# Kernel tuning notes

Hardware: AMD Instinct MI355X
Metric: run time of the kernel (lower is better)

The kernel has to match this reference:

```python
import jax, jax.numpy as jnp
import numpy as np

D_MODEL = 1024
HEAD = 16


def setup_inputs() -> dict:
    key = jax.random.key(0)
    ks = jax.random.split(key, 11)
    B, S, D = 2, 2048, D_MODEL
    s = 1.0 / np.sqrt(D)
    return {
        "query": jax.random.normal(ks[0], (B, S, D), jnp.float32),
        "value": jax.random.normal(ks[1], (B, S, D), jnp.float32),
        "key": jax.random.normal(ks[2], (B, S, D), jnp.float32),
        "Wq_w": jax.random.normal(ks[3], (D, D), jnp.float32) * s,
        "Wq_b": jnp.zeros((D,), jnp.float32),
        "Wk_w": jax.random.normal(ks[4], (D, D), jnp.float32) * s,
        "Wk_b": jnp.zeros((D,), jnp.float32),
        "Wv_w": jax.random.normal(ks[5], (D, D), jnp.float32) * s,
        "Wv_b": jnp.zeros((D,), jnp.float32),
        "Wo_w": jax.random.normal(ks[6], (D, D), jnp.float32) * s,
        "Wo_b": jnp.zeros((D,), jnp.float32),
    }


def reference(query, value, key, Wq_w, Wq_b, Wk_w, Wk_b, Wv_w, Wv_b, Wo_w, Wo_b):
    B, S, D = query.shape
    H = HEAD
    kd = D // H
    # Linear projections (torch Linear: x @ W.T + b)
    Q = query @ Wq_w.T + Wq_b
    K = key @ Wk_w.T + Wk_b
    V = value @ Wv_w.T + Wv_b
    # [B, S, D] -> [B, H, S, kd]
    Q = Q.reshape(B, S, H, kd).transpose(0, 2, 1, 3)
    K = K.reshape(B, S, H, kd).transpose(0, 2, 1, 3)
    V = V.reshape(B, S, H, kd).transpose(0, 2, 1, 3)
    scale = 1.0 / jnp.sqrt(jnp.asarray(kd, query.dtype))
    score = jnp.einsum("bhqd,bhkd->bhqk", Q, K) * scale  # [B,H,S,S]
    attn = jax.nn.softmax(score, axis=-1)
    x = jnp.einsum("bhqk,bhkd->bhqd", attn, V)  # [B,H,S,kd]
    x = x.transpose(0, 2, 1, 3).reshape(B, S, D)
    return x @ Wo_w.T + Wo_b
```

## Files before the change

### kernel.cpp

```cpp
#include <hip/hip_runtime.h>
#include <stdint.h>
#include <stddef.h>


typedef __attribute__((ext_vector_type(8))) short short8;
typedef __attribute__((ext_vector_type(4))) float floatx4;
typedef __attribute__((ext_vector_type(16))) float f32x16;
typedef __attribute__((ext_vector_type(4))) unsigned short ushort4v;

#define MFMA16(a, b, c) __builtin_amdgcn_mfma_f32_16x16x32_bf16((a), (b), (c), 0, 0, 0)
#define MFMA32(a, b, c) __builtin_amdgcn_mfma_f32_32x32x16_bf16((a), (b), (c), 0, 0, 0)

#define CL2 0.18033688011112042f

__device__ __forceinline__ unsigned short f2bf(float f) {
  union { float f; unsigned u; } v; v.f = f;
  unsigned u = v.u;
  return (unsigned short)((u + 0x7fffu + ((u >> 16) & 1u)) >> 16);
}

__device__ __forceinline__ float fast_exp2(float x) {
  float r;
  asm("v_exp_f32 %0, %1" : "=v"(r) : "v"(x));
  return r;
}

__device__ __forceinline__ unsigned cvt_pk_bf16(float lo, float hi) {
  unsigned r;
  asm("v_cvt_pk_bf16_f32 %0, %1, %2" : "=v"(r) : "v"(lo), "v"(hi));
  return r;
}

#define PSWAP(a, b) asm("v_permlane32_swap_b32 %0, %1" : "+v"(a), "+v"(b))

#define WAITBAR(N) do { \
  asm volatile("s_waitcnt vmcnt(" #N ")" ::: "memory"); \
  __builtin_amdgcn_s_barrier(); \
  __builtin_amdgcn_sched_barrier(0); \
} while (0)

union B8 { unsigned short s[8]; short8 v; };
union U4 { unsigned w[4]; short8 v; };

__device__ __forceinline__ void gload_lds16(const unsigned short* g, unsigned short* l) {
  __builtin_amdgcn_global_load_lds(
      (__attribute__((address_space(1))) void*)(g),
      (__attribute__((address_space(3))) void*)(l), 16, 0, 0);
}

__global__ __launch_bounds__(256) void convert_all(
    const float* __restrict__ q, const float* __restrict__ k, const float* __restrict__ v,
    const float* __restrict__ wq, const float* __restrict__ wk,
    const float* __restrict__ wv, const float* __restrict__ wo,
    unsigned short* __restrict__ qb, unsigned short* __restrict__ kb,
    unsigned short* __restrict__ vb, unsigned short* __restrict__ w4)
{
  int b = blockIdx.x;
  const float* s; unsigned short* d;
  float sc = 1.0f;
  if (b < 2048)      { s = q;  d = qb; }
  else if (b < 4096) { s = k;  d = kb; b -= 2048; }
  else if (b < 6144) { s = v;  d = vb; b -= 4096; }
  else if (b < 6656) { s = wq; d = w4;            b -= 6144; sc = CL2; }
  else if (b < 7168) { s = wk; d = w4 + 1048576;  b -= 6656; }
  else if (b < 7680) { s = wv; d = w4 + 2097152;  b -= 7168; }
  else               { s = wo; d = w4 + 3145728;  b -= 7680; }
  const size_t i = ((size_t)b * 256 + threadIdx.x) * 8;
  float4 f0 = *(const float4*)(s + i);
  float4 f1 = *(const float4*)(s + i + 4);
  B8 u;
  u.s[0] = f2bf(f0.x * sc); u.s[1] = f2bf(f0.y * sc);
  u.s[2] = f2bf(f0.z * sc); u.s[3] = f2bf(f0.w * sc);
  u.s[4] = f2bf(f1.x * sc); u.s[5] = f2bf(f1.y * sc);
  u.s[6] = f2bf(f1.z * sc); u.s[7] = f2bf(f1.w * sc);
  *(short8*)(d + i) = u.v;
}

__global__ __launch_bounds__(256) void proj_gemm(
    const unsigned short* __restrict__ A0, const unsigned short* __restrict__ A1,
    const unsigned short* __restrict__ A2, const unsigned short* __restrict__ W4,
    const float* __restrict__ b0, const float* __restrict__ b1, const float* __restrict__ b2,
    unsigned short* __restrict__ Qp, unsigned short* __restrict__ Kp,
    unsigned short* __restrict__ Vt)
{
  const int z = blockIdx.z;
  const unsigned short* A = (z == 0) ? A0 : ((z == 1) ? A1 : A2);
  const unsigned short* W = W4 + (size_t)z * 1048576;
  const float* bias = (z == 0) ? b0 : ((z == 1) ? b1 : b2);
  const float esc = (z == 0) ? CL2 : 1.0f;

  const int m0 = blockIdx.y * 128;
  const int n0 = blockIdx.x * 128;
  const int tid = threadIdx.x;
  const int lane = tid & 63;
  const int wid = tid >> 6;
  const int wr = wid >> 1, wc = wid & 1;
  const int g = lane >> 4, l15 = lane & 15;

  __shared__ unsigned short As[3][128 * 32];
  __shared__ unsigned short Bs[3][128 * 32];

  const floatx4 vzero = {0.f, 0.f, 0.f, 0.f};
  floatx4 acc[4][4];
#pragma unroll
  for (int i = 0; i < 4; ++i)
#pragma unroll
    for (int j = 0; j < 4; ++j) acc[i][j] = vzero;

  const int lr = lane >> 2;
  const int rb0 = wid * 16, rb1 = (4 + wid) * 16;
  const int gsw0 = ((lane & 3) ^ (((rb0 + lr) >> 1) & 3)) * 8;
  const int gsw1 = ((lane & 3) ^ (((rb1 + lr) >> 1) & 3)) * 8;
  const unsigned short* pa0 = &A[(size_t)(m0 + rb0 + lr) * 1024 + gsw0];
  const unsigned short* pa1 = &A[(size_t)(m0 + rb1 + lr) * 1024 + gsw1];
  const unsigned short* pw0 = &W[(size_t)(n0 + rb0 + lr) * 1024 + gsw0];
  const unsigned short* pw1 = &W[(size_t)(n0 + rb1 + lr) * 1024 + gsw1];

#define PSTAGE(s_, b_) do { \
    gload_lds16(pa0 + (s_) * 32, &As[b_][rb0 * 32]); \
    gload_lds16(pa1 + (s_) * 32, &As[b_][rb1 * 32]); \
    gload_lds16(pw0 + (s_) * 32, &Bs[b_][rb0 * 32]); \
    gload_lds16(pw1 + (s_) * 32, &Bs[b_][rb1 * 32]); \
  } while (0)

  PSTAGE(0, 0);
  PSTAGE(1, 1);

  int cur = 0;
  for (int s = 0; s < 32; ++s) {
    if (s < 31) WAITBAR(4); else WAITBAR(0);
    if (s + 2 < 32) {
      int nb = cur + 2; if (nb >= 3) nb -= 3;
      PSTAGE(s + 2, nb);
    }

    short8 af[4], bfr[4];
#pragma unroll
    for (int mt = 0; mt < 4; ++mt) {
      const int R = wr * 64 + mt * 16 + l15;
      af[mt] = *(const short8*)&As[cur][R * 32 + ((g ^ ((R >> 1) & 3)) * 8)];
    }
#pragma unroll
    for (int nt = 0; nt < 4; ++nt) {
      const int R = wc * 64 + nt * 16 + l15;
      bfr[nt] = *(const short8*)&Bs[cur][R * 32 + ((g ^ ((R >> 1) & 3)) * 8)];
    }

    __builtin_amdgcn_s_setprio(1);
#pragma unroll
    for (int mt = 0; mt < 4; ++mt)
#pragma unroll
      for (int nt = 0; nt < 4; ++nt)
        acc[mt][nt] = MFMA16(af[mt], bfr[nt], acc[mt][nt]);
    __builtin_amdgcn_s_setprio(0);

    cur = (cur + 1 == 3) ? 0 : cur + 1;
  }
#undef PSTAGE

  float bvv[4];
#pragma unroll
  for (int nt = 0; nt < 4; ++nt) bvv[nt] = bias[n0 + wc * 64 + nt * 16 + l15] * esc;

  if (z < 2) {
    unsigned short* dst = (z == 0) ? Qp : Kp;
#pragma unroll
    for (int mt = 0; mt < 4; ++mt)
#pragma unroll
      for (int r = 0; r < 4; ++r) {
        const size_t row = (size_t)(m0 + wr * 64 + mt * 16 + g * 4 + r);
#pragma unroll
        for (int nt = 0; nt < 4; ++nt)
          dst[row * 1024 + n0 + wc * 64 + nt * 16 + l15] =
              f2bf(acc[mt][nt][r] + bvv[nt]);
      }
  } else {
#pragma unroll
    for (int mt = 0; mt < 4; ++mt) {
      const int sr = m0 + wr * 64 + mt * 16 + g * 4;
      const int bb = sr >> 11;
      const int ss = sr & 2047;
#pragma unroll
      for (int nt = 0; nt < 4; ++nt) {
        const int n = n0 + wc * 64 + nt * 16 + l15;
        const int hh = n >> 6, dd = n & 63;
        ushort4v o;
#pragma unroll
        for (int r = 0; r < 4; ++r) o[r] = f2bf(acc[mt][nt][r] + bvv[nt]);
        *(ushort4v*)&Vt[((size_t)(bb * 16 + hh) * 64 + dd) * 2048 + ss] = o;
      }
    }
  }
}

__global__ __launch_bounds__(256, 2) void attn_kernel(
    const unsigned short* __restrict__ Qp, const unsigned short* __restrict__ Kp,
    const unsigned short* __restrict__ Vt, unsigned short* __restrict__ X)
{
  const int qb = blockIdx.x;
  const int bh = blockIdx.y;
  const int b = bh >> 4, h = bh & 15;
  const int tid = threadIdx.x, lane = tid & 63, w = tid >> 6;
  const int l31 = lane & 31, hi = lane >> 5;

  __shared__ unsigned short KV[2][2][4096];

  const int qrow = b * 2048 + qb * 128 + w * 32 + l31;
  short8 Qf[4];
#pragma unroll
  for (int ks = 0; ks < 4; ++ks)
    Qf[ks] = *(const short8*)&Qp[(size_t)qrow * 1024 + h * 64 + ks * 16 + hi * 8];

  const int s0 = tid, s1 = tid + 256;
  const int r0 = s0 >> 3, g0 = (s0 & 7) ^ (r0 & 7);
  const int r1 = s1 >> 3, g1 = (s1 & 7) ^ (r1 & 7);
  const unsigned short* kq0 = Kp + (size_t)(b * 2048 + r0) * 1024 + h * 64 + g0 * 8;
  const unsigned short* kq1 = Kp + (size_t)(b * 2048 + r1) * 1024 + h * 64 + g1 * 8;
  const unsigned short* vq0 = Vt + (size_t)(bh * 64 + r0) * 2048 + g0 * 8;
  const unsigned short* vq1 = Vt + (size_t)(bh * 64 + r1) * 2048 + g1 * 8;
  const int db0 = (w * 64) * 8;
  const int db1 = (256 + w * 64) * 8;

  f32x16 o0a, o0b, o1a, o1b;
#pragma unroll
  for (int i = 0; i < 16; ++i) { o0a[i] = 0.f; o0b[i] = 0.f; o1a[i] = 0.f; o1b[i] = 0.f; }
  float lp4[4] = {0.f, 0.f, 0.f, 0.f};

  gload_lds16(kq0, &KV[0][0][db0]);
  gload_lds16(kq1, &KV[0][0][db1]);
  gload_lds16(vq0, &KV[0][1][db0]);
  gload_lds16(vq1, &KV[0][1][db1]);
  __syncthreads();

  int cur = 0;
  for (int t = 0; t < 32; ++t) {
    if (t + 1 < 32) {
      const size_t ko = (size_t)(t + 1) * 65536;
      const size_t vo = (size_t)(t + 1) * 64;
      gload_lds16(kq0 + ko, &KV[cur ^ 1][0][db0]);
      gload_lds16(kq1 + ko, &KV[cur ^ 1][0][db1]);
      gload_lds16(vq0 + vo, &KV[cur ^ 1][1][db0]);
      gload_lds16(vq1 + vo, &KV[cur ^ 1][1][db1]);
    }
    const unsigned short* Kb = &KV[cur][0][0];
    const unsigned short* Vb = &KV[cur][1][0];

    f32x16 c0a, c0b, c1a, c1b;
#pragma unroll
    for (int i = 0; i < 16; ++i) { c0a[i] = 0.f; c0b[i] = 0.f; c1a[i] = 0.f; c1b[i] = 0.f; }
    {
      const int kx = l31 & 7;
      const int base0 = l31 * 64;
      const int base1 = (32 + l31) * 64;
      short8 kf00 = *(const short8*)&Kb[base0 + (((0 + hi) ^ kx) << 3)];
      short8 kf01 = *(const short8*)&Kb[base0 + (((2 + hi) ^ kx) << 3)];
      short8 kf02 = *(const short8*)&Kb[base0 + (((4 + hi) ^ kx) << 3)];
      short8 kf03 = *(const short8*)&Kb[base0 + (((6 + hi) ^ kx) << 3)];
      short8 kf10 = *(const short8*)&Kb[base1 + (((0 + hi) ^ kx) << 3)];
      short8 kf11 = *(const short8*)&Kb[base1 + (((2 + hi) ^ kx) << 3)];
      short8 kf12 = *(const short8*)&Kb[base1 + (((4 + hi) ^ kx) << 3)];
      short8 kf13 = *(const short8*)&Kb[base1 + (((6 + hi) ^ kx) << 3)];
      __builtin_amdgcn_s_setprio(1);
      c0a = MFMA32(kf00, Qf[0], c0a); c0a = MFMA32(kf01, Qf[1], c0a);
      c0b = MFMA32(kf02, Qf[2], c0b); c0b = MFMA32(kf03, Qf[3], c0b);
      c1a = MFMA32(kf10, Qf[0], c1a); c1a = MFMA32(kf11, Qf[1], c1a);
      c1b = MFMA32(kf12, Qf[2], c1b); c1b = MFMA32(kf13, Qf[3], c1b);
      __builtin_amdgcn_s_setprio(0);
    }

    short8 vf0[4], vf1[4];
    {
      const int kx = l31 & 7;
      const int vrow1 = 32 + l31;
#pragma unroll
      for (int ks = 0; ks < 4; ++ks) {
        vf0[ks] = *(const short8*)&Vb[l31 * 64 + (((ks * 2 + hi) ^ kx) << 3)];
        vf1[ks] = *(const short8*)&Vb[vrow1 * 64 + (((ks * 2 + hi) ^ (vrow1 & 7)) << 3)];
      }
    }

#pragma unroll
    for (int i = 0; i < 16; ++i) {
      const float p = fast_exp2(c0a[i] + c0b[i]);
      c0a[i] = p; lp4[i & 3] += p;
    }
#pragma unroll
    for (int i = 0; i < 16; ++i) {
      const float p = fast_exp2(c1a[i] + c1b[i]);
      c1a[i] = p; lp4[i & 3] += p;
    }

    short8 PA0, PA1, PA2, PA3;
    {
      unsigned p0 = cvt_pk_bf16(c0a[0], c0a[1]),   p1 = cvt_pk_bf16(c0a[2], c0a[3]);
      unsigned p2 = cvt_pk_bf16(c0a[4], c0a[5]),   p3 = cvt_pk_bf16(c0a[6], c0a[7]);
      unsigned p4 = cvt_pk_bf16(c0a[8], c0a[9]),   p5 = cvt_pk_bf16(c0a[10], c0a[11]);
      unsigned p6 = cvt_pk_bf16(c0a[12], c0a[13]), p7 = cvt_pk_bf16(c0a[14], c0a[15]);
      PSWAP(p0, p2); PSWAP(p1, p3); PSWAP(p4, p6); PSWAP(p5, p7);
      U4 a_, b_;
      a_.w[0] = p0; a_.w[1] = p1; a_.w[2] = p2; a_.w[3] = p3;      PA0 = a_.v;
      b_.w[0] = p4; b_.w[1] = p5; b_.w[2] = p6; b_.w[3] = p7;      PA1 = b_.v;
    }
    {
      unsigned p0 = cvt_pk_bf16(c1a[0], c1a[1]),   p1 = cvt_pk_bf16(c1a[2], c1a[3]);
      unsigned p2 = cvt_pk_bf16(c1a[4], c1a[5]),   p3 = cvt_pk_bf16(c1a[6], c1a[7]);
      unsigned p4 = cvt_pk_bf16(c1a[8], c1a[9]),   p5 = cvt_pk_bf16(c1a[10], c1a[11]);
      unsigned p6 = cvt_pk_bf16(c1a[12], c1a[13]), p7 = cvt_pk_bf16(c1a[14], c1a[15]);
      PSWAP(p0, p2); PSWAP(p1, p3); PSWAP(p4, p6); PSWAP(p5, p7);
      U4 a_, b_;
      a_.w[0] = p0; a_.w[1] = p1; a_.w[2] = p2; a_.w[3] = p3;      PA2 = a_.v;
      b_.w[0] = p4; b_.w[1] = p5; b_.w[2] = p6; b_.w[3] = p7;      PA3 = b_.v;
    }

    __builtin_amdgcn_s_setprio(1);
    o0a = MFMA32(vf0[0], PA0, o0a); o0a = MFMA32(vf0[1], PA1, o0a);
    o0b = MFMA32(vf0[2], PA2, o0b); o0b = MFMA32(vf0[3], PA3, o0b);
    o1a = MFMA32(vf1[0], PA0, o1a); o1a = MFMA32(vf1[1], PA1, o1a);
    o1b = MFMA32(vf1[2], PA2, o1b); o1b = MFMA32(vf1[3], PA3, o1b);
    __builtin_amdgcn_s_setprio(0);

    __syncthreads();
    cur ^= 1;
  }

  const float l_run = (lp4[0] + lp4[1]) + (lp4[2] + lp4[3]);
  const float l_tot = l_run + __shfl_xor(l_run, 32);
  const float linv = 1.f / l_tot;
#pragma unroll
  for (int a = 0; a < 4; ++a) {
    ushort4v v0, v1;
#pragma unroll
    for (int r = 0; r < 4; ++r) {
      v0[r] = f2bf((o0a[a * 4 + r] + o0b[a * 4 + r]) * linv);
      v1[r] = f2bf((o1a[a * 4 + r] + o1b[a * 4 + r]) * linv);
    }
    *(ushort4v*)&X[(size_t)qrow * 1024 + h * 64 + a * 8 + hi * 4] = v0;
    *(ushort4v*)&X[(size_t)qrow * 1024 + h * 64 + 32 + a * 8 + hi * 4] = v1;
  }
}

__global__ __launch_bounds__(256) void out_gemm(
    const unsigned short* __restrict__ A, const unsigned short* __restrict__ W,
    const float* __restrict__ bias, float* __restrict__ out)
{
  const int m0 = blockIdx.y * 64;
  const int n0 = blockIdx.x * 128;
  const int tid = threadIdx.x;
  const int lane = tid & 63;
  const int wid = tid >> 6;
  const int wr = wid >> 1, wc = wid & 1;
  const int g = lane >> 4, l15 = lane & 15;

  __shared__ unsigned short As[3][64 * 32];
  __shared__ unsigned short Bs[3][128 * 32];

  const floatx4 vzero = {0.f, 0.f, 0.f, 0.f};
  floatx4 acc[2][4];
#pragma unroll
  for (int i = 0; i < 2; ++i)
#pragma unroll
    for (int j = 0; j < 4; ++j) acc[i][j] = vzero;

  const int lr = lane >> 2;
  const int rb0 = wid * 16, rb1 = (4 + wid) * 16;
  const int gsw0 = ((lane & 3) ^ (((rb0 + lr) >> 1) & 3)) * 8;
  const int gsw1 = ((lane & 3) ^ (((rb1 + lr) >> 1) & 3)) * 8;
  const unsigned short* pa0 = &A[(size_t)(m0 + rb0 + lr) * 1024 + gsw0];
  const unsigned short* pw0 = &W[(size_t)(n0 + rb0 + lr) * 1024 + gsw0];
  const unsigned short* pw1 = &W[(size_t)(n0 + rb1 + lr) * 1024 + gsw1];

#define OSTAGE(s_, b_) do { \
    gload_lds16(pa0 + (s_) * 32, &As[b_][rb0 * 32]); \
    gload_lds16(pw0 + (s_) * 32, &Bs[b_][rb0 * 32]); \
    gload_lds16(pw1 + (s_) * 32, &Bs[b_][rb1 * 32]); \
  } while (0)

  OSTAGE(0, 0);
  OSTAGE(1, 1);

  int cur = 0;
  for (int s = 0; s < 32; ++s) {
    if (s < 31) WAITBAR(3); else WAITBAR(0);
    if (s + 2 < 32) {
      int nb = cur + 2; if (nb >= 3) nb -= 3;
      OSTAGE(s + 2, nb);
    }

    short8 af[2], bfr[4];
#pragma unroll
    for (int mt = 0; mt < 2; ++mt) {
      const int R = wr * 32 + mt * 16 + l15;
      af[mt] = *(const short8*)&As[cur][R * 32 + ((g ^ ((R >> 1) & 3)) * 8)];
    }
#pragma unroll
    for (int nt = 0; nt < 4; ++nt) {
      const int R = wc * 64 + nt * 16 + l15;
      bfr[nt] = *(const short8*)&Bs[cur][R * 32 + ((g ^ ((R >> 1) & 3)) * 8)];
    }

    __builtin_amdgcn_s_setprio(1);
#pragma unroll
    for (int mt = 0; mt < 2; ++mt)
#pragma unroll
      for (int nt = 0; nt < 4; ++nt)
        acc[mt][nt] = MFMA16(af[mt], bfr[nt], acc[mt][nt]);
    __builtin_amdgcn_s_setprio(0);

    cur = (cur + 1 == 3) ? 0 : cur + 1;
  }
#undef OSTAGE

  float bvv[4];
#pragma unroll
  for (int nt = 0; nt < 4; ++nt) bvv[nt] = bias[n0 + wc * 64 + nt * 16 + l15];

#pragma unroll
  for (int mt = 0; mt < 2; ++mt)
#pragma unroll
    for (int r = 0; r < 4; ++r) {
      const size_t row = (size_t)(m0 + wr * 32 + mt * 16 + g * 4 + r);
#pragma unroll
      for (int nt = 0; nt < 4; ++nt)
        out[row * 1024 + n0 + wc * 64 + nt * 16 + l15] = acc[mt][nt][r] + bvv[nt];
    }
}

extern "C" void kernel_launch(void* const* d_in, const int* in_sizes, int n_in,
                              void* d_out, int out_size, void* d_ws, size_t ws_size,
                              hipStream_t stream)
{
  const float* query = (const float*)d_in[0];
  const float* value = (const float*)d_in[1];
  const float* key   = (const float*)d_in[2];
  const float* Wq = (const float*)d_in[3];
  const float* bq = (const float*)d_in[4];
  const float* Wk = (const float*)d_in[5];
  const float* bk = (const float*)d_in[6];
  const float* Wv = (const float*)d_in[7];
  const float* bv = (const float*)d_in[8];
  const float* Wo = (const float*)d_in[9];
  const float* bo = (const float*)d_in[10];
  float* out = (float*)d_out;

  const size_t M4 = (size_t)4096 * 1024;
  unsigned short* vb = (unsigned short*)d_ws;
  unsigned short* w4 = vb + M4;
  unsigned short* Qp = w4 + M4;
  unsigned short* Kp = Qp + M4;
  unsigned short* Vt = Kp + M4;
  unsigned short* X  = vb;
  unsigned short* qb = (unsigned short*)d_out;
  unsigned short* kb = qb + M4;

  dim3 blk(256);
  convert_all<<<8192, blk, 0, stream>>>(query, key, value, Wq, Wk, Wv, Wo,
                                        qb, kb, vb, w4);
  proj_gemm<<<dim3(8, 32, 3), blk, 0, stream>>>(qb, kb, vb, w4,
                                                bq, bk, bv, Qp, Kp, Vt);
  attn_kernel<<<dim3(16, 32), blk, 0, stream>>>(Qp, Kp, Vt, X);
  out_gemm<<<dim3(8, 64), blk, 0, stream>>>(X, w4 + 3 * 1048576, bo, out);
}
```

Measured before the change: 124.2 us.

## Load K/V fragments directly from global memory instead of LDS double-buffering

Removes the shared-memory double buffer and async global-to-LDS copies for K and V in the attention kernel. Each wave now reads its MFMA operand fragments straight from global memory every iteration, which also drops the per-iteration block barrier. This gives up sharing across the four waves (each wave re-reads the same K/V tile, relying on L1/L2) and loses prefetch overlap, so load latency is exposed on the critical path.

```diff
diff --git a/kernel.cpp b/kernel.cpp
--- a/kernel.cpp
+++ b/kernel.cpp
@@ -203,80 +203,50 @@
   const int tid = threadIdx.x, lane = tid & 63, w = tid >> 6;
   const int l31 = lane & 31, hi = lane >> 5;
 
-  __shared__ unsigned short KV[2][2][4096];
-
   const int qrow = b * 2048 + qb * 128 + w * 32 + l31;
   short8 Qf[4];
 #pragma unroll
   for (int ks = 0; ks < 4; ++ks)
     Qf[ks] = *(const short8*)&Qp[(size_t)qrow * 1024 + h * 64 + ks * 16 + hi * 8];
 
-  const int s0 = tid, s1 = tid + 256;
-  const int r0 = s0 >> 3, g0 = (s0 & 7) ^ (r0 & 7);
-  const int r1 = s1 >> 3, g1 = (s1 & 7) ^ (r1 & 7);
-  const unsigned short* kq0 = Kp + (size_t)(b * 2048 + r0) * 1024 + h * 64 + g0 * 8;
-  const unsigned short* kq1 = Kp + (size_t)(b * 2048 + r1) * 1024 + h * 64 + g1 * 8;
-  const unsigned short* vq0 = Vt + (size_t)(bh * 64 + r0) * 2048 + g0 * 8;
-  const unsigned short* vq1 = Vt + (size_t)(bh * 64 + r1) * 2048 + g1 * 8;
-  const int db0 = (w * 64) * 8;
-  const int db1 = (256 + w * 64) * 8;
+  const unsigned short* pK0 = Kp + (size_t)(b * 2048 + l31) * 1024 + h * 64 + hi * 8;
+  const unsigned short* pK1 = pK0 + (size_t)32 * 1024;
+  const unsigned short* pV0 = Vt + (size_t)(bh * 64 + l31) * 2048 + hi * 8;
+  const unsigned short* pV1 = pV0 + (size_t)32 * 2048;
 
   f32x16 o0a, o0b, o1a, o1b;
 #pragma unroll
   for (int i = 0; i < 16; ++i) { o0a[i] = 0.f; o0b[i] = 0.f; o1a[i] = 0.f; o1b[i] = 0.f; }
   float lp4[4] = {0.f, 0.f, 0.f, 0.f};
 
-  gload_lds16(kq0, &KV[0][0][db0]);
-  gload_lds16(kq1, &KV[0][0][db1]);
-  gload_lds16(vq0, &KV[0][1][db0]);
-  gload_lds16(vq1, &KV[0][1][db1]);
-  __syncthreads();
-
-  int cur = 0;
   for (int t = 0; t < 32; ++t) {
-    if (t + 1 < 32) {
-      const size_t ko = (size_t)(t + 1) * 65536;
-      const size_t vo = (size_t)(t + 1) * 64;
-      gload_lds16(kq0 + ko, &KV[cur ^ 1][0][db0]);
-      gload_lds16(kq1 + ko, &KV[cur ^ 1][0][db1]);
-      gload_lds16(vq0 + vo, &KV[cur ^ 1][1][db0]);
-      gload_lds16(vq1 + vo, &KV[cur ^ 1][1][db1]);
-    }
-    const unsigned short* Kb = &KV[cur][0][0];
-    const unsigned short* Vb = &KV[cur][1][0];
+    const size_t ko = (size_t)t * 65536;
+    const size_t vo = (size_t)t * 64;
+
+    short8 kf00 = *(const short8*)(pK0 + ko);
+    short8 kf01 = *(const short8*)(pK0 + ko + 16);
+    short8 kf02 = *(const short8*)(pK0 + ko + 32);
+    short8 kf03 = *(const short8*)(pK0 + ko + 48);
+    short8 kf10 = *(const short8*)(pK1 + ko);
+    short8 kf11 = *(const short8*)(pK1 + ko + 16);
+    short8 kf12 = *(const short8*)(pK1 + ko + 32);
+    short8 kf13 = *(const short8*)(pK1 + ko + 48);
 
     f32x16 c0a, c0b, c1a, c1b;
 #pragma unroll
     for (int i = 0; i < 16; ++i) { c0a[i] = 0.f; c0b[i] = 0.f; c1a[i] = 0.f; c1b[i] = 0.f; }
-    {
-      const int kx = l31 & 7;
-      const int base0 = l31 * 64;
-      const int base1 = (32 + l31) * 64;
-      short8 kf00 = *(const short8*)&Kb[base0 + (((0 + hi) ^ kx) << 3)];
-      short8 kf01 = *(const short8*)&Kb[base0 + (((2 + hi) ^ kx) << 3)];
-      short8 kf02 = *(const short8*)&Kb[base0 + (((4 + hi) ^ kx) << 3)];
-      short8 kf03 = *(const short8*)&Kb[base0 + (((6 + hi) ^ kx) << 3)];
-      short8 kf10 = *(const short8*)&Kb[base1 + (((0 + hi) ^ kx) << 3)];
-      short8 kf11 = *(const short8*)&Kb[base1 + (((2 + hi) ^ kx) << 3)];
-      short8 kf12 = *(const short8*)&Kb[base1 + (((4 + hi) ^ kx) << 3)];
-      short8 kf13 = *(const short8*)&Kb[base1 + (((6 + hi) ^ kx) << 3)];
-      __builtin_amdgcn_s_setprio(1);
-      c0a = MFMA32(kf00, Qf[0], c0a); c0a = MFMA32(kf01, Qf[1], c0a);
-      c0b = MFMA32(kf02, Qf[2], c0b); c0b = MFMA32(kf03, Qf[3], c0b);
-      c1a = MFMA32(kf10, Qf[0], c1a); c1a = MFMA32(kf11, Qf[1], c1a);
-      c1b = MFMA32(kf12, Qf[2], c1b); c1b = MFMA32(kf13, Qf[3], c1b);
-      __builtin_amdgcn_s_setprio(0);
-    }
+    __builtin_amdgcn_s_setprio(1);
+    c0a = MFMA32(kf00, Qf[0], c0a); c0a = MFMA32(kf01, Qf[1], c0a);
+    c0b = MFMA32(kf02, Qf[2], c0b); c0b = MFMA32(kf03, Qf[3], c0b);
+    c1a = MFMA32(kf10, Qf[0], c1a); c1a = MFMA32(kf11, Qf[1], c1a);
+    c1b = MFMA32(kf12, Qf[2], c1b); c1b = MFMA32(kf13, Qf[3], c1b);
+    __builtin_amdgcn_s_setprio(0);
 
     short8 vf0[4], vf1[4];
-    {
-      const int kx = l31 & 7;
-      const int vrow1 = 32 + l31;
-#pragma unroll
-      for (int ks = 0; ks < 4; ++ks) {
-        vf0[ks] = *(const short8*)&Vb[l31 * 64 + (((ks * 2 + hi) ^ kx) << 3)];
-        vf1[ks] = *(const short8*)&Vb[vrow1 * 64 + (((ks * 2 + hi) ^ (vrow1 & 7)) << 3)];
-      }
+#pragma unroll
+    for (int ks = 0; ks < 4; ++ks) {
+      vf0[ks] = *(const short8*)(pV0 + vo + ks * 16);
+      vf1[ks] = *(const short8*)(pV1 + vo + ks * 16);
     }
 
 #pragma unroll
@@ -318,9 +288,6 @@
     o1a = MFMA32(vf1[0], PA0, o1a); o1a = MFMA32(vf1[1], PA1, o1a);
     o1b = MFMA32(vf1[2], PA2, o1b); o1b = MFMA32(vf1[3], PA3, o1b);
     __builtin_amdgcn_s_setprio(0);
-
-    __syncthreads();
-    cur ^= 1;
   }
 
   const float l_run = (lp4[0] + lp4[1]) + (lp4[2] + lp4[3]);
```

Result: slower. 193.7 us (+56.0%).

## Switch projection GEMMs to BK=64 double-buffered LDS pipeline with 8-way swizzle

Applied to the files above, without the earlier changes.

The QKV-projection and output-projection GEMMs now stage K-tiles of 64 instead of 32, using two LDS buffers instead of three, with a new XOR swizzle over 8 column groups and a cooperative whole-block load pattern. The explicit vmcnt-plus-barrier wait is replaced by __syncthreads at the end of each iteration, and there are half as many iterations. The aim is fewer barriers per unit of MFMA work and more MFMAs between synchronizations. In exchange the prefetch distance drops from two stages to one, and the plain __syncthreads may rely on the compiler to insert the correct waits for global_load_lds, which could expose load latency.

```diff
diff --git a/kernel.cpp b/kernel.cpp
--- a/kernel.cpp
+++ b/kernel.cpp
@@ -32,12 +32,6 @@
 }
 
 #define PSWAP(a, b) asm("v_permlane32_swap_b32 %0, %1" : "+v"(a), "+v"(b))
-
-#define WAITBAR(N) do { \
-  asm volatile("s_waitcnt vmcnt(" #N ")" ::: "memory"); \
-  __builtin_amdgcn_s_barrier(); \
-  __builtin_amdgcn_sched_barrier(0); \
-} while (0)
 
 union B8 { unsigned short s[8]; short8 v; };
 union U4 { unsigned w[4]; short8 v; };
@@ -97,8 +91,8 @@
   const int wr = wid >> 1, wc = wid & 1;
   const int g = lane >> 4, l15 = lane & 15;
 
-  __shared__ unsigned short As[3][128 * 32];
-  __shared__ unsigned short Bs[3][128 * 32];
+  __shared__ unsigned short As[2][128 * 64];
+  __shared__ unsigned short Bs[2][128 * 64];
 
   const floatx4 vzero = {0.f, 0.f, 0.f, 0.f};
   floatx4 acc[4][4];
@@ -107,54 +101,67 @@
 #pragma unroll
     for (int j = 0; j < 4; ++j) acc[i][j] = vzero;
 
-  const int lr = lane >> 2;
-  const int rb0 = wid * 16, rb1 = (4 + wid) * 16;
-  const int gsw0 = ((lane & 3) ^ (((rb0 + lr) >> 1) & 3)) * 8;
-  const int gsw1 = ((lane & 3) ^ (((rb1 + lr) >> 1) & 3)) * 8;
-  const unsigned short* pa0 = &A[(size_t)(m0 + rb0 + lr) * 1024 + gsw0];
-  const unsigned short* pa1 = &A[(size_t)(m0 + rb1 + lr) * 1024 + gsw1];
-  const unsigned short* pw0 = &W[(size_t)(n0 + rb0 + lr) * 1024 + gsw0];
-  const unsigned short* pw1 = &W[(size_t)(n0 + rb1 + lr) * 1024 + gsw1];
-
-#define PSTAGE(s_, b_) do { \
-    gload_lds16(pa0 + (s_) * 32, &As[b_][rb0 * 32]); \
-    gload_lds16(pa1 + (s_) * 32, &As[b_][rb1 * 32]); \
-    gload_lds16(pw0 + (s_) * 32, &Bs[b_][rb0 * 32]); \
-    gload_lds16(pw1 + (s_) * 32, &Bs[b_][rb1 * 32]); \
+  int srow[4], sgr[4];
+#pragma unroll
+  for (int e = 0; e < 4; ++e) {
+    const int slot = e * 256 + tid;
+    srow[e] = slot >> 3;
+    sgr[e] = ((slot & 7) ^ (srow[e] & 7)) * 8;
+  }
+  const unsigned short* paA[4];
+  const unsigned short* paW[4];
+#pragma unroll
+  for (int e = 0; e < 4; ++e) {
+    paA[e] = &A[(size_t)(m0 + srow[e]) * 1024 + sgr[e]];
+    paW[e] = &W[(size_t)(n0 + srow[e]) * 1024 + sgr[e]];
+  }
+  const int wdb = (tid >> 6) * 64 * 8;
+
+#define PSTAGE(k0_, b_) do { \
+    _Pragma("unroll") \
+    for (int e = 0; e < 4; ++e) { \
+      gload_lds16(paA[e] + (k0_), &As[b_][(e * 256 + (tid & ~63)) * 8]); \
+      gload_lds16(paW[e] + (k0_), &Bs[b_][(e * 256 + (tid & ~63)) * 8]); \
+    } \
   } while (0)
 
   PSTAGE(0, 0);
-  PSTAGE(1, 1);
+  __syncthreads();
 
   int cur = 0;
-  for (int s = 0; s < 32; ++s) {
-    if (s < 31) WAITBAR(4); else WAITBAR(0);
-    if (s + 2 < 32) {
-      int nb = cur + 2; if (nb >= 3) nb -= 3;
-      PSTAGE(s + 2, nb);
-    }
-
-    short8 af[4], bfr[4];
+  for (int s = 0; s < 16; ++s) {
+    if (s + 1 < 16) PSTAGE((s + 1) * 64, cur ^ 1);
+
+    short8 af[4][2], bfr[4][2];
 #pragma unroll
     for (int mt = 0; mt < 4; ++mt) {
       const int R = wr * 64 + mt * 16 + l15;
-      af[mt] = *(const short8*)&As[cur][R * 32 + ((g ^ ((R >> 1) & 3)) * 8)];
+      const int rx = R & 7;
+#pragma unroll
+      for (int ks = 0; ks < 2; ++ks)
+        af[mt][ks] = *(const short8*)&As[cur][R * 64 + (((ks * 4 + g) ^ rx) << 3)];
     }
 #pragma unroll
     for (int nt = 0; nt < 4; ++nt) {
       const int R = wc * 64 + nt * 16 + l15;
-      bfr[nt] = *(const short8*)&Bs[cur][R * 32 + ((g ^ ((R >> 1) & 3)) * 8)];
+      const int rx = R & 7;
+#pragma unroll
+      for (int ks = 0; ks < 2; ++ks)
+        bfr[nt][ks] = *(const short8*)&Bs[cur][R * 64 + (((ks * 4 + g) ^ rx) << 3)];
     }
 
     __builtin_amdgcn_s_setprio(1);
 #pragma unroll
-    for (int mt = 0; mt < 4; ++mt)
-#pragma unroll
-      for (int nt = 0; nt < 4; ++nt)
-        acc[mt][nt] = MFMA16(af[mt], bfr[nt], acc[mt][nt]);
+    for (int ks = 0; ks < 2; ++ks)
+#pragma unroll
+      for (int mt = 0; mt < 4; ++mt)
+#pragma unroll
+        for (int nt = 0; nt < 4; ++nt)
+          acc[mt][nt] = MFMA16(af[mt][ks], bfr[nt][ks], acc[mt][nt]);
     __builtin_amdgcn_s_setprio(0);
 
-    cur = (cur + 1 == 3) ? 0 : cur + 1;
+    __syncthreads();
+    cur ^= 1;
   }
 #undef PSTAGE
 
@@ -351,8 +358,8 @@
   const int wr = wid >> 1, wc = wid & 1;
   const int g = lane >> 4, l15 = lane & 15;
 
-  __shared__ unsigned short As[3][64 * 32];
-  __shared__ unsigned short Bs[3][128 * 32];
+  __shared__ unsigned short As[2][64 * 64];
+  __shared__ unsigned short Bs[2][128 * 64];
 
   const floatx4 vzero = {0.f, 0.f, 0.f, 0.f};
   floatx4 acc[2][4];
@@ -361,52 +368,73 @@
 #pragma unroll
     for (int j = 0; j < 4; ++j) acc[i][j] = vzero;
 
-  const int lr = lane >> 2;
-  const int rb0 = wid * 16, rb1 = (4 + wid) * 16;
-  const int gsw0 = ((lane & 3) ^ (((rb0 + lr) >> 1) & 3)) * 8;
-  const int gsw1 = ((lane & 3) ^ (((rb1 + lr) >> 1) & 3)) * 8;
-  const unsigned short* pa0 = &A[(size_t)(m0 + rb0 + lr) * 1024 + gsw0];
-  const unsigned short* pw0 = &W[(size_t)(n0 + rb0 + lr) * 1024 + gsw0];
-  const unsigned short* pw1 = &W[(size_t)(n0 + rb1 + lr) * 1024 + gsw1];
-
-#define OSTAGE(s_, b_) do { \
-    gload_lds16(pa0 + (s_) * 32, &As[b_][rb0 * 32]); \
-    gload_lds16(pw0 + (s_) * 32, &Bs[b_][rb0 * 32]); \
-    gload_lds16(pw1 + (s_) * 32, &Bs[b_][rb1 * 32]); \
+  int arow[2], agr[2];
+#pragma unroll
+  for (int e = 0; e < 2; ++e) {
+    const int slot = e * 256 + tid;
+    arow[e] = slot >> 3;
+    agr[e] = ((slot & 7) ^ (arow[e] & 7)) * 8;
+  }
+  int brow[4], bgr[4];
+#pragma unroll
+  for (int e = 0; e < 4; ++e) {
+    const int slot = e * 256 + tid;
+    brow[e] = slot >> 3;
+    bgr[e] = ((slot & 7) ^ (brow[e] & 7)) * 8;
+  }
+  const unsigned short* paA[2];
+  const unsigned short* paW[4];
+#pragma unroll
+  for (int e = 0; e < 2; ++e) paA[e] = &A[(size_t)(m0 + arow[e]) * 1024 + agr[e]];
+#pragma unroll
+  for (int e = 0; e < 4; ++e) paW[e] = &W[(size_t)(n0 + brow[e]) * 1024 + bgr[e]];
+
+#define OSTAGE(k0_, b_) do { \
+    _Pragma("unroll") \
+    for (int e = 0; e < 2; ++e) \
+      gload_lds16(paA[e] + (k0_), &As[b_][(e * 256 + (tid & ~63)) * 8]); \
+    _Pragma("unroll") \
+    for (int e = 0; e < 4; ++e) \
+      gload_lds16(paW[e] + (k0_), &Bs[b_][(e * 256 + (tid & ~63)) * 8]); \
   } while (0)
 
   OSTAGE(0, 0);
-  OSTAGE(1, 1);
+  __syncthreads();
 
   int cur = 0;
-  for (int s = 0; s < 32; ++s) {
-    if (s < 31) WAITBAR(3); else WAITBAR(0);
-    if (s + 2 < 32) {
-      int nb = cur + 2; if (nb >= 3) nb -= 3;
-      OSTAGE(s + 2, nb);
-    }
-
-    short8 af[2], bfr[4];
+  for (int s = 0; s < 16; ++s) {
+    if (s + 1 < 16) OSTAGE((s + 1) * 64, cur ^ 1);
+
+    short8 af[2][2], bfr[4][2];
 #pragma unroll
     for (int mt = 0; mt < 2; ++mt) {
       const int R = wr * 32 + mt * 16 + l15;
-      af[mt] = *(const short8*)&As[cur][R * 32 + ((g ^ ((R >> 1) & 3)) * 8)];
+      const int rx = R & 7;
+#pragma unroll
+      for (int ks = 0; ks < 2; ++ks)
+        af[mt][ks] = *(const short8*)&As[cur][R * 64 + (((ks * 4 + g) ^ rx) << 3)];
     }
 #pragma unroll
     for (int nt = 0; nt < 4; ++nt) {
       const int R = wc * 64 + nt * 16 + l15;
-      bfr[nt] = *(const short8*)&Bs[cur][R * 32 + ((g ^ ((R >> 1) & 3)) * 8)];
+      const int rx = R & 7;
+#pragma unroll
+      for (int ks = 0; ks < 2; ++ks)
+        bfr[nt][ks] = *(const short8*)&Bs[cur][R * 64 + (((ks * 4 + g) ^ rx) << 3)];
     }
 
     __builtin_amdgcn_s_setprio(1);
 #pragma unroll
-    for (int mt = 0; mt < 2; ++mt)
-#pragma unroll
-      for (int nt = 0; nt < 4; ++nt)
-        acc[mt][nt] = MFMA16(af[mt], bfr[nt], acc[mt][nt]);
+    for (int ks = 0; ks < 2; ++ks)
+#pragma unroll
+      for (int mt = 0; mt < 2; ++mt)
+#pragma unroll
+        for (int nt = 0; nt < 4; ++nt)
+          acc[mt][nt] = MFMA16(af[mt][ks], bfr[nt][ks], acc[mt][nt]);
     __builtin_amdgcn_s_setprio(0);
 
-    cur = (cur + 1 == 3) ? 0 : cur + 1;
+    __syncthreads();
+    cur ^= 1;
   }
 #undef OSTAGE
 
```

Measured after the change: 129.5 us. +4.3%, slower.
